# Kernel optimization log

Hardware: AMD Instinct MI355X
Metric: run time of the kernel (lower is better)

## Reference

```python
import jax, jax.numpy as jnp
import numpy as np

R = 25          # regions (hard-coded [:25, 0] slice in the source)
NUM_CONSUMER = 27


def _ln(x, g, b, axes, eps):
    m = jnp.mean(x, axis=axes, keepdims=True)
    v = jnp.mean((x - m) ** 2, axis=axes, keepdims=True)
    return (x - m) / jnp.sqrt(v + eps) * g + b


def setup_inputs() -> dict:
    key = jax.random.key(0)
    n, c, h, e = 64, 64, 8, 1024
    bs = R
    ks = jax.random.split(key, 24)
    inp = {
        "business_structure_target": jax.random.normal(ks[0], (bs, c, n, 4), jnp.float32),
        "business_structure_infected": jax.random.normal(ks[1], (bs, c, n, 4), jnp.float32),
        "customer_structure_target": jax.random.uniform(ks[2], (bs, c, n, NUM_CONSUMER, 4), jnp.float32),
        "customer_structure_infected": jax.random.uniform(ks[3], (bs, c, n, NUM_CONSUMER, 4), jnp.float32),
        "index_target_idx": jax.random.randint(ks[4], (bs, c), 0, R, jnp.int32),
        "index_infected_idx": jax.random.randint(ks[5], (bs, c), 0, R, jnp.int32),
        "covid_outbreak_business": jax.random.randint(ks[6], (bs, c), 0, n, jnp.int32),
        # parameters
        "emb_weight": jax.random.normal(ks[7], (R * n, e), jnp.float32),
        "emb_ln_g": jnp.ones((e,), jnp.float32),
        "emb_ln_b": jnp.zeros((e,), jnp.float32),
        "WQ_t": jax.random.normal(ks[8], (h, e, e), jnp.float32) / np.sqrt(e),
        "WK_t": jax.random.normal(ks[9], (h, e, e), jnp.float32) / np.sqrt(e),
        "WQ_i": jax.random.normal(ks[10], (h, e, e), jnp.float32) / np.sqrt(e),
        "WK_i": jax.random.normal(ks[11], (h, e, e), jnp.float32) / np.sqrt(e),
        "W_os": jax.random.normal(ks[12], (e, e), jnp.float32) / np.sqrt(e),
        "b_os": jnp.zeros((e,), jnp.float32),
        "BS_g": jnp.ones((c, n), jnp.float32), "BS_b": jnp.zeros((c, n), jnp.float32),
        "CS_g": jnp.ones((c, n), jnp.float32), "CS_b": jnp.zeros((c, n), jnp.float32),
        "OS_g": jnp.ones((c, n), jnp.float32), "OS_b": jnp.zeros((c, n), jnp.float32),
    }
    return inp


def _mha(emb_blocks, WQ, WK, indices):
    # emb_blocks: (R, n, e); indices: (d,)
    d = indices.shape[0]
    n, e = emb_blocks.shape[1], emb_blocks.shape[2]
    ew = emb_blocks[indices].reshape(d * n, e)           # gather district blocks
    Q = jnp.einsum('te,hfe->htf', ew, WQ).reshape(-1, d, n, e)  # torch Linear: x @ W.T
    K = jnp.einsum('te,hfe->htf', ew, WK).reshape(-1, d, n, e)
    QK = jnp.einsum('hdie,hdje->hdij', Q, K) / jnp.sqrt(jnp.float32(e))
    # torch Softmax(dim=1) on (d, n, n) -> normalize over the first industry axis
    return jax.nn.softmax(QK, axis=2)                    # (h, d, n, n)


def reference(business_structure_target, business_structure_infected,
              customer_structure_target, customer_structure_infected,
              index_target_idx, index_infected_idx, covid_outbreak_business,
              emb_weight, emb_ln_g, emb_ln_b,
              WQ_t, WK_t, WQ_i, WK_i, W_os, b_os,
              BS_g, BS_b, CS_g, CS_b, OS_g, OS_b):
    n = business_structure_target.shape[2]
    e = emb_weight.shape[1]

    bt = jnp.mean(business_structure_target, -1)[:R, 0]      # (R, n)
    bi = jnp.mean(business_structure_infected, -1)[0]        # (c, n)
    ct = jnp.mean(customer_structure_target, -1)[:R, 0]      # (R, n, 27)
    ci = jnp.mean(customer_structure_infected, -1)[0]        # (c, n, 27)

    emb_norm = _ln(emb_weight, emb_ln_g, emb_ln_b, -1, 1e-16)
    emb_blocks = emb_norm.reshape(R, n, e)

    idx_t = index_target_idx[:R, 0].astype(jnp.int32)        # (R,)
    idx_i = index_infected_idx[0].astype(jnp.int32)          # (c,)

    attn_t = _mha(emb_blocks, WQ_t, WK_t, idx_t)             # (h, R, n, n)
    BR_trg = jnp.einsum('di,hdij->djh', bt, attn_t)          # (R, n, h)
    attn_i = _mha(emb_blocks, WQ_i, WK_i, idx_i)             # (h, c, n, n)
    BR_inf = jnp.einsum('di,hdij->djh', bi, attn_i)          # (c, n, h)

    # cosine similarity over the head dim, broadcast (R,1,n,h) x (1,c,n,h)
    eps = 1e-15
    a = BR_trg[:, None]
    b = BR_inf[None]
    dot = jnp.sum(a * b, -1)
    na = jnp.maximum(jnp.sqrt(jnp.sum(a * a, -1)), eps)
    nb = jnp.maximum(jnp.sqrt(jnp.sum(b * b, -1)), eps)
    BS = dot / (na * nb)                                     # (R, c, n)

    # JSD-style customer-structure similarity
    lt = jax.nn.log_softmax(ct, -1)[:, None]                 # (R, 1, n, 27)
    li = jax.nn.log_softmax(ci, -1)[None]                    # (1, c, n, 27)
    M = jax.nn.log_softmax((lt + li) / 2, -1)
    expM = jnp.exp(M)
    # KLDivLoss(log_target=True): exp(target) * (target - input)
    kl_t = jnp.mean(expM * (M - lt), -1)
    kl_i = jnp.mean(expM * (M - li), -1)
    CS = -((kl_t + kl_i) / 2)                                # (R, c, n)

    # outbreak-business similarity
    cov_buz = covid_outbreak_business[0].astype(jnp.int32)   # (c,)
    inf_emb_idx = idx_i * n + cov_buz
    ob_emb = emb_weight[inf_emb_idx] @ W_os.T + b_os         # (c, e)
    OS = (ob_emb @ emb_weight.T).reshape(-1, R, n)           # (c, R, n)
    OS = jnp.transpose(OS, (1, 0, 2))                        # (R, c, n)

    BS = _ln(BS, BS_g, BS_b, (-2, -1), 1e-5)
    CS = _ln(CS, CS_g, CS_b, (-2, -1), 1e-5)
    OS = _ln(OS, OS_g, OS_b, (-2, -1), 1e-5)
    return (BS, CS, OS)
```

## Files before the change

### kernel.cpp

```cpp
#include <hip/hip_runtime.h>
#include <math.h>

#define RR 25
#define HH 8
#define EE 1024
#define NCN 27

typedef short bf16x8 __attribute__((ext_vector_type(8)));
typedef float f32x4 __attribute__((ext_vector_type(4)));
typedef unsigned short us4 __attribute__((ext_vector_type(4)));
typedef unsigned short us8 __attribute__((ext_vector_type(8)));

__device__ __forceinline__ unsigned short f2bf(float x) {
    union { float f; unsigned int u; } v; v.f = x;
    const unsigned int u = v.u;
    return (unsigned short)((u + 0x7fffu + ((u >> 16) & 1u)) >> 16);
}
__device__ __forceinline__ float bf2f(unsigned short h) {
    union { unsigned int u; float f; } v; v.u = ((unsigned int)h) << 16;
    return v.f;
}

__device__ __forceinline__ float block_reduce_sum_256(float v, float* red) {
#pragma unroll
    for (int off = 32; off > 0; off >>= 1) v += __shfl_down(v, off, 64);
    const int lane = threadIdx.x & 63, wid = threadIdx.x >> 6;
    if (lane == 0) red[wid] = v;
    __syncthreads();
    if (threadIdx.x == 0) red[0] = red[0] + red[1] + red[2] + red[3];
    __syncthreads();
    const float r = red[0];
    __syncthreads();
    return r;
}

__global__ __launch_bounds__(256) void k_ln_emb(
    const float* __restrict__ emb, const float* __restrict__ g,
    const float* __restrict__ b, float* __restrict__ out,
    unsigned short* __restrict__ eh, unsigned short* __restrict__ el)
{
    __shared__ float red[4];
    const int t = blockIdx.x;
    const float* row = emb + (size_t)t * EE;
    float4 x = reinterpret_cast<const float4*>(row)[threadIdx.x];
    float s = x.x + x.y + x.z + x.w;
    s = block_reduce_sum_256(s, red);
    const float m = s * (1.0f / 1024.0f);
    const float d0 = x.x - m, d1 = x.y - m, d2 = x.z - m, d3 = x.w - m;
    float sq = d0*d0 + d1*d1 + d2*d2 + d3*d3;
    sq = block_reduce_sum_256(sq, red);
    const float rs = rsqrtf(sq * (1.0f / 1024.0f) + 1e-16f);
    const float4 gv = reinterpret_cast<const float4*>(g)[threadIdx.x];
    const float4 bv = reinterpret_cast<const float4*>(b)[threadIdx.x];
    float o[4];
    o[0] = d0 * rs * gv.x + bv.x;
    o[1] = d1 * rs * gv.y + bv.y;
    o[2] = d2 * rs * gv.z + bv.z;
    o[3] = d3 * rs * gv.w + bv.w;
    float4 of; of.x = o[0]; of.y = o[1]; of.z = o[2]; of.w = o[3];
    reinterpret_cast<float4*>(out + (size_t)t * EE)[threadIdx.x] = of;
    us4 hv, lv;
#pragma unroll
    for (int j = 0; j < 4; ++j) {
        const unsigned short h = f2bf(o[j]);
        hv[j] = h; lv[j] = f2bf(o[j] - bf2f(h));
    }
    *reinterpret_cast<us4*>(eh + (size_t)t * EE + threadIdx.x * 4) = hv;
    *reinterpret_cast<us4*>(el + (size_t)t * EE + threadIdx.x * 4) = lv;
}

#define WTEN 16777216
#define WPLN 8388608
__global__ __launch_bounds__(256) void k_splitw(
    const float* __restrict__ w0, const float* __restrict__ w1,
    const float* __restrict__ w2, const float* __restrict__ w3,
    unsigned short* __restrict__ wsp)
{
    const int t = blockIdx.y;
    const float* src = (t == 0) ? w0 : ((t == 1) ? w1 : ((t == 2) ? w2 : w3));
    unsigned short* hb = wsp + (size_t)t * WTEN;
    unsigned short* lb = hb + WPLN;
    const size_t q = (size_t)blockIdx.x * 256 + threadIdx.x;
    const float4 x = reinterpret_cast<const float4*>(src)[q];
    const float xf[4] = {x.x, x.y, x.z, x.w};
    us4 hv, lv;
#pragma unroll
    for (int j = 0; j < 4; ++j) {
        const unsigned short h = f2bf(xf[j]);
        hv[j] = h; lv[j] = f2bf(xf[j] - bf2f(h));
    }
    *reinterpret_cast<us4*>(hb + q * 4) = hv;
    *reinterpret_cast<us4*>(lb + q * 4) = lv;
}

struct SplitTiles {
    unsigned short Ah[64][40], Al[64][40], Bh[64][40], Bl[64][40];
};

#define MFMA_COMPUTE(SM)                                                         \
    {                                                                            \
        bf16x8 ah_[2], al_[2], bh_[2], bl_[2];                                   \
        _Pragma("unroll")                                                        \
        for (int m = 0; m < 2; ++m) {                                            \
            const int r = wr * 32 + m * 16 + fr;                                 \
            ah_[m] = *reinterpret_cast<const bf16x8*>(&(SM).Ah[r][ch * 8]);      \
            al_[m] = *reinterpret_cast<const bf16x8*>(&(SM).Al[r][ch * 8]);      \
        }                                                                        \
        _Pragma("unroll")                                                        \
        for (int n = 0; n < 2; ++n) {                                            \
            const int r = wc * 32 + n * 16 + fr;                                 \
            bh_[n] = *reinterpret_cast<const bf16x8*>(&(SM).Bh[r][ch * 8]);      \
            bl_[n] = *reinterpret_cast<const bf16x8*>(&(SM).Bl[r][ch * 8]);      \
        }                                                                        \
        _Pragma("unroll")                                                        \
        for (int m = 0; m < 2; ++m)                                              \
            _Pragma("unroll")                                                    \
            for (int n = 0; n < 2; ++n) {                                        \
                acc[m][n] = __builtin_amdgcn_mfma_f32_16x16x32_bf16(ah_[m], bh_[n], acc[m][n], 0, 0, 0); \
                acc[m][n] = __builtin_amdgcn_mfma_f32_16x16x32_bf16(ah_[m], bl_[n], acc[m][n], 0, 0, 0); \
                acc[m][n] = __builtin_amdgcn_mfma_f32_16x16x32_bf16(al_[m], bh_[n], acc[m][n], 0, 0, 0); \
            }                                                                    \
    }

#define MFMA_STAGE_SPLIT(ABASE, BBASE, SM)                                       \
    {                                                                            \
        float4 ra[2], rb[2];                                                     \
        _Pragma("unroll")                                                        \
        for (int l = 0; l < 2; ++l) {                                            \
            const int id = l * 256 + tid;                                        \
            const int row = id >> 3, c4 = (id & 7) * 4;                          \
            ra[l] = *reinterpret_cast<const float4*>((ABASE) + (size_t)row * EE + k0 + c4); \
            rb[l] = *reinterpret_cast<const float4*>((BBASE) + (size_t)row * EE + k0 + c4); \
        }                                                                        \
        __syncthreads();                                                         \
        _Pragma("unroll")                                                        \
        for (int l = 0; l < 2; ++l) {                                            \
            const int id = l * 256 + tid;                                        \
            const int row = id >> 3, c4 = (id & 7) * 4;                          \
            const float xa[4] = {ra[l].x, ra[l].y, ra[l].z, ra[l].w};            \
            const float xb[4] = {rb[l].x, rb[l].y, rb[l].z, rb[l].w};            \
            us4 ahv, alv, bhv, blv;                                              \
            _Pragma("unroll")                                                    \
            for (int j = 0; j < 4; ++j) {                                        \
                const unsigned short ha = f2bf(xa[j]);                           \
                ahv[j] = ha; alv[j] = f2bf(xa[j] - bf2f(ha));                    \
                const unsigned short hb = f2bf(xb[j]);                           \
                bhv[j] = hb; blv[j] = f2bf(xb[j] - bf2f(hb));                    \
            }                                                                    \
            *reinterpret_cast<us4*>(&(SM).Ah[row][c4]) = ahv;                    \
            *reinterpret_cast<us4*>(&(SM).Al[row][c4]) = alv;                    \
            *reinterpret_cast<us4*>(&(SM).Bh[row][c4]) = bhv;                    \
            *reinterpret_cast<us4*>(&(SM).Bl[row][c4]) = blv;                    \
        }                                                                        \
        __syncthreads();                                                         \
    }

__global__ __launch_bounds__(256) void k_proj_pre(
    const unsigned short* __restrict__ eh, const unsigned short* __restrict__ el,
    const unsigned short* __restrict__ wq, const unsigned short* __restrict__ wk,
    float* __restrict__ Qb, float* __restrict__ Kb, int qkHeadStride)
{
    __shared__ __align__(16) SplitTiles sm;
    const int h = blockIdx.z >> 1;
    const int pk = blockIdx.z & 1;
    const unsigned short* base = pk ? wk : wq;
    const unsigned short* Wh = base + (size_t)h * 1048576;
    const unsigned short* Wl = base + WPLN + (size_t)h * 1048576;
    float* C = (pk ? Kb : Qb) + (size_t)h * qkHeadStride;
    const int bx = blockIdx.x, by = blockIdx.y;
    const int tid = threadIdx.x;
    const int lane = tid & 63, w = tid >> 6;
    const int wr = w >> 1, wc = w & 1;
    const int fr = lane & 15, ch = lane >> 4;
    const int srow = tid >> 2, c8 = (tid & 3) * 8;
    const unsigned short* Ah_src = eh + ((size_t)(by * 64 + srow)) * EE + c8;
    const unsigned short* Al_src = el + ((size_t)(by * 64 + srow)) * EE + c8;
    const unsigned short* Bh_src = Wh + ((size_t)(bx * 64 + srow)) * EE + c8;
    const unsigned short* Bl_src = Wl + ((size_t)(bx * 64 + srow)) * EE + c8;
    f32x4 acc[2][2] = {};
    for (int k0 = 0; k0 < EE; k0 += 32) {
        const us8 va = *reinterpret_cast<const us8*>(Ah_src + k0);
        const us8 vb = *reinterpret_cast<const us8*>(Al_src + k0);
        const us8 vc = *reinterpret_cast<const us8*>(Bh_src + k0);
        const us8 vd = *reinterpret_cast<const us8*>(Bl_src + k0);
        __syncthreads();
        *reinterpret_cast<us8*>(&sm.Ah[srow][c8]) = va;
        *reinterpret_cast<us8*>(&sm.Al[srow][c8]) = vb;
        *reinterpret_cast<us8*>(&sm.Bh[srow][c8]) = vc;
        *reinterpret_cast<us8*>(&sm.Bl[srow][c8]) = vd;
        __syncthreads();
        MFMA_COMPUTE(sm)
    }
    const int rg = lane >> 4;
#pragma unroll
    for (int m = 0; m < 2; ++m)
#pragma unroll
        for (int n = 0; n < 2; ++n)
#pragma unroll
            for (int q = 0; q < 4; ++q) {
                const int row = by * 64 + wr * 32 + m * 16 + rg * 4 + q;
                const int col = bx * 64 + wc * 32 + n * 16 + fr;
                C[(size_t)row * EE + col] = acc[m][n][q];
            }
}

__global__ __launch_bounds__(256) void k_proj_mfma(
    const float* __restrict__ A,
    const float* __restrict__ WQ, const float* __restrict__ WK,
    float* __restrict__ Qb, float* __restrict__ Kb, int qkHeadStride)
{
    __shared__ __align__(16) SplitTiles sm;
    const int h = blockIdx.z >> 1;
    const int pk = blockIdx.z & 1;
    const float* W = (pk ? WK : WQ) + (size_t)h * EE * EE;
    float* C = (pk ? Kb : Qb) + (size_t)h * qkHeadStride;
    const int bx = blockIdx.x, by = blockIdx.y;
    const int tid = threadIdx.x;
    const int lane = tid & 63, w = tid >> 6;
    const int wr = w >> 1, wc = w & 1;
    const int fr = lane & 15, ch = lane >> 4;
    const float* Abase = A + (size_t)by * 64 * EE;
    const float* Bbase = W + (size_t)bx * 64 * EE;
    f32x4 acc[2][2] = {};
    for (int k0 = 0; k0 < EE; k0 += 32) {
        MFMA_STAGE_SPLIT(Abase, Bbase, sm)
        MFMA_COMPUTE(sm)
    }
    const int rg = lane >> 4;
#pragma unroll
    for (int m = 0; m < 2; ++m)
#pragma unroll
        for (int n = 0; n < 2; ++n)
#pragma unroll
            for (int q = 0; q < 4; ++q) {
                const int row = by * 64 + wr * 32 + m * 16 + rg * 4 + q;
                const int col = bx * 64 + wc * 32 + n * 16 + fr;
                C[(size_t)row * EE + col] = acc[m][n][q];
            }
}

__global__ __launch_bounds__(256) void k_qk_mfma(
    const float* __restrict__ Qall, const float* __restrict__ Kall,
    float* __restrict__ attn_all, int qkHeadStride, int attnHeadStride)
{
    __shared__ __align__(16) union { SplitTiles t; float Ss[64][65]; } u;
    __shared__ float redm[4][64];
    __shared__ float reds[4][64];
    const int r = blockIdx.x;
    const int h = blockIdx.y;
    const float* Q = Qall + (size_t)h * qkHeadStride;
    const float* K = Kall + (size_t)h * qkHeadStride;
    float* attn = attn_all + (size_t)h * attnHeadStride + (size_t)r * 4096;
    const int tid = threadIdx.x;
    const int lane = tid & 63, w = tid >> 6;
    const int wr = w >> 1, wc = w & 1;
    const int fr = lane & 15, ch = lane >> 4;
    const float* Abase = Q + (size_t)r * 64 * EE;
    const float* Bbase = K + (size_t)r * 64 * EE;
    f32x4 acc[2][2] = {};
    for (int k0 = 0; k0 < EE; k0 += 32) {
        MFMA_STAGE_SPLIT(Abase, Bbase, u.t)
        MFMA_COMPUTE(u.t)
    }
    __syncthreads();
    const int rg = lane >> 4;
#pragma unroll
    for (int m = 0; m < 2; ++m)
#pragma unroll
        for (int n = 0; n < 2; ++n)
#pragma unroll
            for (int q = 0; q < 4; ++q)
                u.Ss[wr * 32 + m * 16 + rg * 4 + q][wc * 32 + n * 16 + fr] =
                    acc[m][n][q] * (1.0f / 32.0f);
    __syncthreads();
    const int j = tid & 63, seg = tid >> 6;
    float mx = -1e30f;
#pragma unroll
    for (int i = 0; i < 16; ++i) mx = fmaxf(mx, u.Ss[seg * 16 + i][j]);
    redm[seg][j] = mx;
    __syncthreads();
    const float cm = fmaxf(fmaxf(redm[0][j], redm[1][j]), fmaxf(redm[2][j], redm[3][j]));
    float ssum = 0.f;
#pragma unroll
    for (int i = 0; i < 16; ++i) {
        const float e = __expf(u.Ss[seg * 16 + i][j] - cm);
        u.Ss[seg * 16 + i][j] = e;
        ssum += e;
    }
    reds[seg][j] = ssum;
    __syncthreads();
    const float inv = 1.0f / (reds[0][j] + reds[1][j] + reds[2][j] + reds[3][j]);
#pragma unroll
    for (int i = 0; i < 16; ++i)
        attn[(seg * 16 + i) * 64 + j] = u.Ss[seg * 16 + i][j] * inv;
}

#define GEMM_INNER()                                                            \
    _Pragma("unroll 8")                                                         \
    for (int kk = 0; kk < 32; ++kk) {                                           \
        const float a0 = As[ty4+0][kk], a1 = As[ty4+1][kk],                     \
                    a2 = As[ty4+2][kk], a3 = As[ty4+3][kk];                     \
        const float b0 = Bs[tx4+0][kk], b1 = Bs[tx4+1][kk],                     \
                    b2 = Bs[tx4+2][kk], b3 = Bs[tx4+3][kk];                     \
        acc[0][0] += a0*b0; acc[0][1] += a0*b1; acc[0][2] += a0*b2; acc[0][3] += a0*b3; \
        acc[1][0] += a1*b0; acc[1][1] += a1*b1; acc[1][2] += a1*b2; acc[1][3] += a1*b3; \
        acc[2][0] += a2*b0; acc[2][1] += a2*b1; acc[2][2] += a2*b2; acc[2][3] += a2*b3; \
        acc[3][0] += a3*b0; acc[3][1] += a3*b1; acc[3][2] += a3*b2; acc[3][3] += a3*b3; \
    }

#define GEMM_LOAD_TILES(ABASE, BBASE)                                           \
    _Pragma("unroll")                                                           \
    for (int l = 0; l < 2; ++l) {                                               \
        const int idx = l * 256 + tid;                                          \
        const int row = idx >> 3, seg = (idx & 7) * 4;                          \
        const float4 va = *reinterpret_cast<const float4*>((ABASE) + (size_t)row * EE + k0 + seg); \
        As[row][seg+0] = va.x; As[row][seg+1] = va.y;                           \
        As[row][seg+2] = va.z; As[row][seg+3] = va.w;                           \
        const float4 vb = *reinterpret_cast<const float4*>((BBASE) + (size_t)row * EE + k0 + seg); \
        Bs[row][seg+0] = vb.x; Bs[row][seg+1] = vb.y;                           \
        Bs[row][seg+2] = vb.z; Bs[row][seg+3] = vb.w;                           \
    }

__global__ __launch_bounds__(64) void k_br(
    const float* __restrict__ bst, const float* __restrict__ bsi,
    const int* __restrict__ iti, const int* __restrict__ iii,
    const float* __restrict__ attn_t, const float* __restrict__ attn_i,
    float* __restrict__ br_t, float* __restrict__ br_i)
{
    __shared__ float bw[64];
    const int dp = blockIdx.x;
    const int h = blockIdx.y;
    const int j = threadIdx.x;
    const float* attn;
    float* out;
    if (dp < RR) {
        const int d = dp;
        const int rb = iti[d * 64];
        const float* p = bst + ((size_t)(d * 64) * 64 + j) * 4;
        bw[j] = 0.25f * (p[0] + p[1] + p[2] + p[3]);
        attn = attn_t + ((size_t)h * RR + rb) * 4096;
        out = br_t + (size_t)d * 64 * 8;
    } else {
        const int d = dp - RR;
        const int rb = iii[d];
        const float* p = bsi + ((size_t)d * 64 + j) * 4;
        bw[j] = 0.25f * (p[0] + p[1] + p[2] + p[3]);
        attn = attn_i + ((size_t)h * RR + rb) * 4096;
        out = br_i + (size_t)d * 64 * 8;
    }
    __syncthreads();
    float acc = 0.f;
#pragma unroll 8
    for (int i = 0; i < 64; ++i) acc += bw[i] * attn[i * 64 + j];
    out[(size_t)j * 8 + h] = acc;
}

__global__ __launch_bounds__(256) void k_norms(
    const float* __restrict__ br_t, const float* __restrict__ br_i,
    float* __restrict__ na, float* __restrict__ nb)
{
    const int t = blockIdx.x * 256 + threadIdx.x;
    if (t < 1600) {
        float s = 0.f;
#pragma unroll
        for (int h = 0; h < 8; ++h) { const float v = br_t[(size_t)t*8 + h]; s += v*v; }
        na[t] = fmaxf(sqrtf(s), 1e-15f);
    } else if (t < 1600 + 4096) {
        const int u = t - 1600;
        float s = 0.f;
#pragma unroll
        for (int h = 0; h < 8; ++h) { const float v = br_i[(size_t)u*8 + h]; s += v*v; }
        nb[u] = fmaxf(sqrtf(s), 1e-15f);
    }
}

__global__ __launch_bounds__(256) void k_bs(
    const float* __restrict__ br_t, const float* __restrict__ br_i,
    const float* __restrict__ na, const float* __restrict__ nb,
    float* __restrict__ raw)
{
    const int p = blockIdx.x;
#pragma unroll
    for (int it = 0; it < 16; ++it) {
        const int o = it * 256 + threadIdx.x;
        const int q = o >> 6, j = o & 63;
        const float* a = br_t + ((size_t)p * 64 + j) * 8;
        const float* b = br_i + ((size_t)q * 64 + j) * 8;
        float dot = 0.f;
#pragma unroll
        for (int h = 0; h < 8; ++h) dot += a[h] * b[h];
        raw[(size_t)p * 4096 + o] = dot / (na[p * 64 + j] * nb[q * 64 + j]);
    }
}

__global__ __launch_bounds__(256) void k_lsm(
    const float* __restrict__ cst, const float* __restrict__ csi,
    float* __restrict__ lt, float* __restrict__ li)
{
    const int row = blockIdx.x * 256 + threadIdx.x;
    if (row >= 1600 + 4096) return;
    const float* src;
    float* dst;
    if (row < 1600) {
        const int d = row >> 6, i = row & 63;
        src = cst + ((size_t)(d * 64) * 64 + i) * NCN * 4;
        dst = lt + (size_t)row * NCN;
    } else {
        const int u = row - 1600;
        const int q = u >> 6, i = u & 63;
        src = csi + ((size_t)q * 64 + i) * NCN * 4;
        dst = li + (size_t)u * NCN;
    }
    float x[NCN];
    float m = -1e30f;
#pragma unroll
    for (int k = 0; k < NCN; ++k) {
        x[k] = 0.25f * (src[k*4] + src[k*4+1] + src[k*4+2] + src[k*4+3]);
        m = fmaxf(m, x[k]);
    }
    float s = 0.f;
#pragma unroll
    for (int k = 0; k < NCN; ++k) s += __expf(x[k] - m);
    const float lse = m + __logf(s);
#pragma unroll
    for (int k = 0; k < NCN; ++k) dst[k] = x[k] - lse;
}

__global__ __launch_bounds__(256) void k_cs(
    const float* __restrict__ lt, const float* __restrict__ li, float* __restrict__ raw)
{
    const int p = blockIdx.x;
    for (int it = 0; it < 16; ++it) {
        const int o = it * 256 + threadIdx.x;
        const int q = o >> 6, i = o & 63;
        const float* a = lt + ((size_t)p * 64 + i) * NCN;
        const float* b = li + ((size_t)q * 64 + i) * NCN;
        float la[NCN], lb[NCN];
        float m = -1e30f;
#pragma unroll
        for (int k = 0; k < NCN; ++k) {
            la[k] = a[k]; lb[k] = b[k];
            m = fmaxf(m, 0.5f * (la[k] + lb[k]));
        }
        float z = 0.f;
#pragma unroll
        for (int k = 0; k < NCN; ++k) z += __expf(0.5f * (la[k] + lb[k]) - m);
        const float lse = m + __logf(z);
        float kt = 0.f, ki = 0.f;
#pragma unroll
        for (int k = 0; k < NCN; ++k) {
            const float M = 0.5f * (la[k] + lb[k]) - lse;
            const float eM = __expf(M);
            kt += eM * (M - la[k]);
            ki += eM * (M - lb[k]);
        }
        raw[(size_t)p * 4096 + o] = -(kt + ki) * (0.5f / 27.0f);
    }
}

__global__ __launch_bounds__(256) void k_obemb(
    const float* __restrict__ emb, const float* __restrict__ Wos,
    const float* __restrict__ bos, const int* __restrict__ iii,
    const int* __restrict__ cob, float* __restrict__ ob)
{
    __shared__ float As[64][33];
    __shared__ float Bs[64][33];
    __shared__ int gidx[64];
    const int bx = blockIdx.x;
    const int tid = threadIdx.x;
    const int tx = tid & 15, ty = tid >> 4;
    const int ty4 = ty * 4, tx4 = tx * 4;
    if (tid < 64) gidx[tid] = iii[tid] * 64 + cob[tid];
    __syncthreads();
    const float* Bbase = Wos + (size_t)bx * 64 * EE;
    float acc[4][4] = {};
    for (int k0 = 0; k0 < EE; k0 += 32) {
#pragma unroll
        for (int l = 0; l < 2; ++l) {
            const int idx = l * 256 + tid;
            const int row = idx >> 3, seg = (idx & 7) * 4;
            const float4 va = *reinterpret_cast<const float4*>(emb + (size_t)gidx[row] * EE + k0 + seg);
            As[row][seg+0] = va.x; As[row][seg+1] = va.y; As[row][seg+2] = va.z; As[row][seg+3] = va.w;
            const float4 vb = *reinterpret_cast<const float4*>(Bbase + (size_t)row * EE + k0 + seg);
            Bs[row][seg+0] = vb.x; Bs[row][seg+1] = vb.y; Bs[row][seg+2] = vb.z; Bs[row][seg+3] = vb.w;
        }
        __syncthreads();
        GEMM_INNER()
        __syncthreads();
    }
#pragma unroll
    for (int q = 0; q < 4; ++q)
#pragma unroll
        for (int r2 = 0; r2 < 4; ++r2)
            ob[(size_t)(ty4 + q) * EE + bx*64 + tx4 + r2] = acc[q][r2] + bos[bx*64 + tx4 + r2];
}

__global__ __launch_bounds__(256) void k_os(
    const float* __restrict__ ob, const float* __restrict__ emb, float* __restrict__ raw)
{
    __shared__ float As[64][33];
    __shared__ float Bs[64][33];
    const int p = blockIdx.x;
    const int tid = threadIdx.x;
    const int tx = tid & 15, ty = tid >> 4;
    const int ty4 = ty * 4, tx4 = tx * 4;
    const float* Abase = ob;
    const float* Bbase = emb + (size_t)p * 64 * EE;
    float acc[4][4] = {};
    for (int k0 = 0; k0 < EE; k0 += 32) {
        GEMM_LOAD_TILES(Abase, Bbase)
        __syncthreads();
        GEMM_INNER()
        __syncthreads();
    }
#pragma unroll
    for (int q = 0; q < 4; ++q)
#pragma unroll
        for (int r2 = 0; r2 < 4; ++r2)
            raw[(size_t)p * 4096 + (ty4 + q) * 64 + tx4 + r2] = acc[q][r2];
}

__global__ __launch_bounds__(256) void k_final_ln(
    const float* __restrict__ raw,
    const float* __restrict__ BSg, const float* __restrict__ BSb,
    const float* __restrict__ CSg, const float* __restrict__ CSb,
    const float* __restrict__ OSg, const float* __restrict__ OSb,
    float* __restrict__ out)
{
    __shared__ float red[4];
    const int s = blockIdx.x, p = blockIdx.y;
    const float* g  = (s == 0) ? BSg : ((s == 1) ? CSg : OSg);
    const float* bb = (s == 0) ? BSb : ((s == 1) ? CSb : OSb);
    const float* x = raw + ((size_t)s * RR + p) * 4096;
    float v[16];
    float sum = 0.f;
#pragma unroll
    for (int it = 0; it < 16; ++it) { v[it] = x[it * 256 + threadIdx.x]; sum += v[it]; }
    sum = block_reduce_sum_256(sum, red);
    const float m = sum * (1.0f / 4096.0f);
    float sq = 0.f;
#pragma unroll
    for (int it = 0; it < 16; ++it) { const float d = v[it] - m; sq += d * d; }
    sq = block_reduce_sum_256(sq, red);
    const float rs = rsqrtf(sq * (1.0f / 4096.0f) + 1e-5f);
    float* o = out + ((size_t)s * RR + p) * 4096;
#pragma unroll
    for (int it = 0; it < 16; ++it) {
        const int oo = it * 256 + threadIdx.x;
        o[oo] = (v[it] - m) * rs * g[oo] + bb[oo];
    }
}

extern "C" void kernel_launch(void* const* d_in, const int* in_sizes, int n_in,
                              void* d_out, int out_size, void* d_ws, size_t ws_size,
                              hipStream_t stream)
{
    const float* bst = (const float*)d_in[0];
    const float* bsi = (const float*)d_in[1];
    const float* cst = (const float*)d_in[2];
    const float* csi = (const float*)d_in[3];
    const int*   iti = (const int*)d_in[4];
    const int*   iii = (const int*)d_in[5];
    const int*   cob = (const int*)d_in[6];
    const float* embw = (const float*)d_in[7];
    const float* eg  = (const float*)d_in[8];
    const float* ebb = (const float*)d_in[9];
    const float* WQt = (const float*)d_in[10];
    const float* WKt = (const float*)d_in[11];
    const float* WQi = (const float*)d_in[12];
    const float* WKi = (const float*)d_in[13];
    const float* Wos = (const float*)d_in[14];
    const float* bos = (const float*)d_in[15];
    const float* BSg = (const float*)d_in[16];
    const float* BSb = (const float*)d_in[17];
    const float* CSg = (const float*)d_in[18];
    const float* CSb = (const float*)d_in[19];
    const float* OSg = (const float*)d_in[20];
    const float* OSb = (const float*)d_in[21];

    const size_t tailF  = 819200ull*2 + 12800 + 32768 + 1600 + 4096 + 43200 + 110592 + 65536 + 307200;
    const size_t baseF  = 1638400ull + 819200 + 819200;
    const size_t wspF   = 33554432ull;
    const size_t qk8F   = 2ull * 8 * 1600 * EE;
    const size_t qk1F   = 2ull * 1600 * EE;
    const size_t needBig = (baseF + wspF + qk8F + tailF) * 4;
    const size_t needMid = (baseF + qk8F + tailF) * 4;
    const int tier = (ws_size >= needBig) ? 2 : ((ws_size >= needMid) ? 1 : 0);

    float* ws = (float*)d_ws;
    size_t cur = 0;
    float* emb_n = ws + cur;                      cur += 1638400;
    unsigned short* emb_h = (unsigned short*)(ws + cur); cur += 819200;
    unsigned short* emb_l = (unsigned short*)(ws + cur); cur += 819200;
    unsigned short* wsp = nullptr;
    if (tier == 2) { wsp = (unsigned short*)(ws + cur); cur += wspF; }
    const size_t qkSz = (tier >= 1) ? (size_t)8 * 1600 * EE : (size_t)1600 * EE;
    float* Qbuf   = ws + cur;        cur += qkSz;
    float* Kbuf   = ws + cur;        cur += qkSz;
    float* attn_t = ws + cur;        cur += 819200;
    float* attn_i = ws + cur;        cur += 819200;
    float* br_t   = ws + cur;        cur += 12800;
    float* br_i   = ws + cur;        cur += 32768;
    float* na     = ws + cur;        cur += 1600;
    float* nb     = ws + cur;        cur += 4096;
    float* lt     = ws + cur;        cur += 43200;
    float* li     = ws + cur;        cur += 110592;
    float* ob     = ws + cur;        cur += 65536;
    float* raw    = ws + cur;        cur += 307200;

    k_ln_emb<<<1600, 256, 0, stream>>>(embw, eg, ebb, emb_n, emb_h, emb_l);
    if (tier == 2)
        k_splitw<<<dim3(8192, 4), 256, 0, stream>>>(WQt, WKt, WQi, WKi, wsp);

    for (int w = 0; w < 2; ++w) {
        const float* WQ = w ? WQi : WQt;
        const float* WK = w ? WKi : WKt;
        float* attn = w ? attn_i : attn_t;
        if (tier == 2) {
            k_proj_pre<<<dim3(16, 25, 16), 256, 0, stream>>>(
                emb_h, emb_l, wsp + (size_t)(2*w) * WTEN, wsp + (size_t)(2*w+1) * WTEN,
                Qbuf, Kbuf, 1600 * EE);
            k_qk_mfma<<<dim3(25, 8), 256, 0, stream>>>(Qbuf, Kbuf, attn, 1600 * EE, RR * 4096);
        } else if (tier == 1) {
            k_proj_mfma<<<dim3(16, 25, 16), 256, 0, stream>>>(emb_n, WQ, WK, Qbuf, Kbuf, 1600 * EE);
            k_qk_mfma<<<dim3(25, 8), 256, 0, stream>>>(Qbuf, Kbuf, attn, 1600 * EE, RR * 4096);
        } else {
            for (int h = 0; h < HH; ++h) {
                k_proj_mfma<<<dim3(16, 25, 2), 256, 0, stream>>>(
                    emb_n, WQ + (size_t)h * EE * EE, WK + (size_t)h * EE * EE, Qbuf, Kbuf, 0);
                k_qk_mfma<<<dim3(25, 1), 256, 0, stream>>>(
                    Qbuf, Kbuf, attn + (size_t)h * RR * 4096, 0, 0);
            }
        }
    }

    k_br<<<dim3(RR + 64, 8), 64, 0, stream>>>(bst, bsi, iti, iii, attn_t, attn_i, br_t, br_i);
    k_norms<<<23, 256, 0, stream>>>(br_t, br_i, na, nb);
    k_bs<<<25, 256, 0, stream>>>(br_t, br_i, na, nb, raw);
    k_lsm<<<23, 256, 0, stream>>>(cst, csi, lt, li);
    k_cs<<<25, 256, 0, stream>>>(lt, li, raw + 102400);
    k_obemb<<<16, 256, 0, stream>>>(embw, Wos, bos, iii, cob, ob);
    k_os<<<25, 256, 0, stream>>>(ob, embw, raw + 204800);
    k_final_ln<<<dim3(3, RR), 256, 0, stream>>>(raw, BSg, BSb, CSg, CSb, OSg, OSb, (float*)d_out);
}
```

Baseline: 969.2 us.

## Pre-swizzle split-bf16 operands into MFMA fragment layout and enlarge projection tiles

The embedding and weight hi/lo bf16 splits are now written directly in per-lane MFMA fragment order. A new projection kernel loads contiguous slabs into LDS with no padding or transposition and computes a 64x256 tile per block, with a block-to-XCD mapping for L2 locality. This targets the operand re-fetch and LDS staging overhead of the dominant Q/K projection GEMMs. It also folds the norm kernel into k_bs and moves the small outbreak GEMMs from scalar FMA to split-bf16 MFMA, which raises register pressure and may lower occupancy.

```diff
diff --git a/kernel.cpp b/kernel.cpp
--- a/kernel.cpp
+++ b/kernel.cpp
@@ -34,10 +34,13 @@
     return r;
 }
 
+#define WTEN 16777216ull
+#define WHEAD 2097152ull
+
 __global__ __launch_bounds__(256) void k_ln_emb(
     const float* __restrict__ emb, const float* __restrict__ g,
     const float* __restrict__ b, float* __restrict__ out,
-    unsigned short* __restrict__ eh, unsigned short* __restrict__ el)
+    unsigned short* __restrict__ Apl)
 {
     __shared__ float red[4];
     const int t = blockIdx.x;
@@ -65,12 +68,14 @@
         const unsigned short h = f2bf(o[j]);
         hv[j] = h; lv[j] = f2bf(o[j] - bf2f(h));
     }
-    *reinterpret_cast<us4*>(eh + (size_t)t * EE + threadIdx.x * 4) = hv;
-    *reinterpret_cast<us4*>(el + (size_t)t * EE + threadIdx.x * 4) = lv;
-}
-
-#define WTEN 16777216
-#define WPLN 8388608
+    const int k0 = threadIdx.x * 4;
+    const int kt = k0 >> 5, kc = (k0 >> 3) & 3, j0 = k0 & 7;
+    const int lane = (t & 15) + 16 * kc;
+    const size_t base = ((size_t)(kt * 100 + (t >> 4)) * 2) * 512 + lane * 8 + j0;
+    *reinterpret_cast<us4*>(Apl + base)       = hv;
+    *reinterpret_cast<us4*>(Apl + base + 512) = lv;
+}
+
 __global__ __launch_bounds__(256) void k_splitw(
     const float* __restrict__ w0, const float* __restrict__ w1,
     const float* __restrict__ w2, const float* __restrict__ w3,
@@ -78,8 +83,7 @@
 {
     const int t = blockIdx.y;
     const float* src = (t == 0) ? w0 : ((t == 1) ? w1 : ((t == 2) ? w2 : w3));
-    unsigned short* hb = wsp + (size_t)t * WTEN;
-    unsigned short* lb = hb + WPLN;
+    unsigned short* dst = wsp + (size_t)t * WTEN;
     const size_t q = (size_t)blockIdx.x * 256 + threadIdx.x;
     const float4 x = reinterpret_cast<const float4*>(src)[q];
     const float xf[4] = {x.x, x.y, x.z, x.w};
@@ -89,8 +93,85 @@
         const unsigned short h = f2bf(xf[j]);
         hv[j] = h; lv[j] = f2bf(xf[j] - bf2f(h));
     }
-    *reinterpret_cast<us4*>(hb + q * 4) = hv;
-    *reinterpret_cast<us4*>(lb + q * 4) = lv;
+    const size_t e4 = q * 4;
+    const int h = (int)(e4 >> 20);
+    const int rem = (int)(e4 & 1048575);
+    const int f = rem >> 10, e = rem & 1023;
+    const int kt = e >> 5, kc = (e >> 3) & 3, j0 = e & 7;
+    const int lane = (f & 15) + 16 * kc;
+    const size_t base = (size_t)h * WHEAD + ((size_t)(kt * 64 + (f >> 4)) * 2) * 512 + lane * 8 + j0;
+    *reinterpret_cast<us4*>(dst + base)       = hv;
+    *reinterpret_cast<us4*>(dst + base + 512) = lv;
+}
+
+__global__ __launch_bounds__(256) void k_proj2(
+    const unsigned short* __restrict__ Apl,
+    const unsigned short* __restrict__ Wpl,
+    float* __restrict__ Qb, float* __restrict__ Kb)
+{
+    __shared__ __align__(16) unsigned short As_l[8 * 512];
+    __shared__ __align__(16) unsigned short Bs_l[32 * 512];
+    const int fid = blockIdx.x;
+    const int xcd = fid & 7;
+    const int iw = fid >> 3;
+    const int z = xcd + (iw / 100) * 8;
+    const int mb = iw % 100;
+    const int by = mb >> 2, bx = mb & 3;
+    const int pk = z >> 3, h = z & 7;
+    const unsigned short* Wb = Wpl + (size_t)pk * WTEN + (size_t)h * WHEAD;
+    float* C = (pk ? Kb : Qb) + (size_t)h * 1600 * EE;
+    const int tid = threadIdx.x;
+    const int lane = tid & 63, wv = tid >> 6;
+    const int by4 = by * 4, bx16 = bx * 16;
+    f32x4 acc[4][4] = {};
+    for (int kt = 0; kt < 32; ++kt) {
+        const unsigned short* aslab = Apl + ((size_t)(kt * 100 + by4)) * 1024;
+        const unsigned short* bslab = Wb  + ((size_t)(kt * 64  + bx16)) * 1024;
+        us8 ra0 = *reinterpret_cast<const us8*>(aslab + (size_t)tid * 8);
+        us8 ra1 = *reinterpret_cast<const us8*>(aslab + (size_t)(256 + tid) * 8);
+        us8 rb[8];
+#pragma unroll
+        for (int c = 0; c < 8; ++c)
+            rb[c] = *reinterpret_cast<const us8*>(bslab + (size_t)(c * 256 + tid) * 8);
+        __syncthreads();
+        *reinterpret_cast<us8*>(As_l + tid * 8) = ra0;
+        *reinterpret_cast<us8*>(As_l + (256 + tid) * 8) = ra1;
+#pragma unroll
+        for (int c = 0; c < 8; ++c)
+            *reinterpret_cast<us8*>(Bs_l + (c * 256 + tid) * 8) = rb[c];
+        __syncthreads();
+        bf16x8 ah[4], al[4], bh[4], bl[4];
+#pragma unroll
+        for (int m = 0; m < 4; ++m) {
+            ah[m] = *reinterpret_cast<const bf16x8*>(As_l + (m * 2 + 0) * 512 + lane * 8);
+            al[m] = *reinterpret_cast<const bf16x8*>(As_l + (m * 2 + 1) * 512 + lane * 8);
+        }
+#pragma unroll
+        for (int n = 0; n < 4; ++n) {
+            const int nt = wv * 4 + n;
+            bh[n] = *reinterpret_cast<const bf16x8*>(Bs_l + (nt * 2 + 0) * 512 + lane * 8);
+            bl[n] = *reinterpret_cast<const bf16x8*>(Bs_l + (nt * 2 + 1) * 512 + lane * 8);
+        }
+#pragma unroll
+        for (int m = 0; m < 4; ++m)
+#pragma unroll
+            for (int n = 0; n < 4; ++n) {
+                acc[m][n] = __builtin_amdgcn_mfma_f32_16x16x32_bf16(ah[m], bh[n], acc[m][n], 0, 0, 0);
+                acc[m][n] = __builtin_amdgcn_mfma_f32_16x16x32_bf16(ah[m], bl[n], acc[m][n], 0, 0, 0);
+                acc[m][n] = __builtin_amdgcn_mfma_f32_16x16x32_bf16(al[m], bh[n], acc[m][n], 0, 0, 0);
+            }
+    }
+    const int rg = lane >> 4, fr = lane & 15;
+#pragma unroll
+    for (int m = 0; m < 4; ++m)
+#pragma unroll
+        for (int n = 0; n < 4; ++n)
+#pragma unroll
+            for (int q = 0; q < 4; ++q) {
+                const int row = by * 64 + m * 16 + rg * 4 + q;
+                const int col = bx * 256 + wv * 64 + n * 16 + fr;
+                C[(size_t)row * EE + col] = acc[m][n][q];
+            }
 }
 
 struct SplitTiles {
@@ -122,15 +203,15 @@
             }                                                                    \
     }
 
-#define MFMA_STAGE_SPLIT(ABASE, BBASE, SM)                                       \
+#define MFMA_STAGE_SPLIT_GEN(AROW, BROW, SM)                                     \
     {                                                                            \
         float4 ra[2], rb[2];                                                     \
         _Pragma("unroll")                                                        \
         for (int l = 0; l < 2; ++l) {                                            \
             const int id = l * 256 + tid;                                        \
             const int row = id >> 3, c4 = (id & 7) * 4;                          \
-            ra[l] = *reinterpret_cast<const float4*>((ABASE) + (size_t)row * EE + k0 + c4); \
-            rb[l] = *reinterpret_cast<const float4*>((BBASE) + (size_t)row * EE + k0 + c4); \
+            ra[l] = *reinterpret_cast<const float4*>((AROW(row)) + k0 + c4);     \
+            rb[l] = *reinterpret_cast<const float4*>((BROW(row)) + k0 + c4);     \
         }                                                                        \
         __syncthreads();                                                         \
         _Pragma("unroll")                                                        \
@@ -155,55 +236,6 @@
         __syncthreads();                                                         \
     }
 
-__global__ __launch_bounds__(256) void k_proj_pre(
-    const unsigned short* __restrict__ eh, const unsigned short* __restrict__ el,
-    const unsigned short* __restrict__ wq, const unsigned short* __restrict__ wk,
-    float* __restrict__ Qb, float* __restrict__ Kb, int qkHeadStride)
-{
-    __shared__ __align__(16) SplitTiles sm;
-    const int h = blockIdx.z >> 1;
-    const int pk = blockIdx.z & 1;
-    const unsigned short* base = pk ? wk : wq;
-    const unsigned short* Wh = base + (size_t)h * 1048576;
-    const unsigned short* Wl = base + WPLN + (size_t)h * 1048576;
-    float* C = (pk ? Kb : Qb) + (size_t)h * qkHeadStride;
-    const int bx = blockIdx.x, by = blockIdx.y;
-    const int tid = threadIdx.x;
-    const int lane = tid & 63, w = tid >> 6;
-    const int wr = w >> 1, wc = w & 1;
-    const int fr = lane & 15, ch = lane >> 4;
-    const int srow = tid >> 2, c8 = (tid & 3) * 8;
-    const unsigned short* Ah_src = eh + ((size_t)(by * 64 + srow)) * EE + c8;
-    const unsigned short* Al_src = el + ((size_t)(by * 64 + srow)) * EE + c8;
-    const unsigned short* Bh_src = Wh + ((size_t)(bx * 64 + srow)) * EE + c8;
-    const unsigned short* Bl_src = Wl + ((size_t)(bx * 64 + srow)) * EE + c8;
-    f32x4 acc[2][2] = {};
-    for (int k0 = 0; k0 < EE; k0 += 32) {
-        const us8 va = *reinterpret_cast<const us8*>(Ah_src + k0);
-        const us8 vb = *reinterpret_cast<const us8*>(Al_src + k0);
-        const us8 vc = *reinterpret_cast<const us8*>(Bh_src + k0);
-        const us8 vd = *reinterpret_cast<const us8*>(Bl_src + k0);
-        __syncthreads();
-        *reinterpret_cast<us8*>(&sm.Ah[srow][c8]) = va;
-        *reinterpret_cast<us8*>(&sm.Al[srow][c8]) = vb;
-        *reinterpret_cast<us8*>(&sm.Bh[srow][c8]) = vc;
-        *reinterpret_cast<us8*>(&sm.Bl[srow][c8]) = vd;
-        __syncthreads();
-        MFMA_COMPUTE(sm)
-    }
-    const int rg = lane >> 4;
-#pragma unroll
-    for (int m = 0; m < 2; ++m)
-#pragma unroll
-        for (int n = 0; n < 2; ++n)
-#pragma unroll
-            for (int q = 0; q < 4; ++q) {
-                const int row = by * 64 + wr * 32 + m * 16 + rg * 4 + q;
-                const int col = bx * 64 + wc * 32 + n * 16 + fr;
-                C[(size_t)row * EE + col] = acc[m][n][q];
-            }
-}
-
 __global__ __launch_bounds__(256) void k_proj_mfma(
     const float* __restrict__ A,
     const float* __restrict__ WQ, const float* __restrict__ WK,
@@ -221,11 +253,15 @@
     const int fr = lane & 15, ch = lane >> 4;
     const float* Abase = A + (size_t)by * 64 * EE;
     const float* Bbase = W + (size_t)bx * 64 * EE;
+#define AROWP(r) (Abase + (size_t)(r) * EE)
+#define BROWP(r) (Bbase + (size_t)(r) * EE)
     f32x4 acc[2][2] = {};
     for (int k0 = 0; k0 < EE; k0 += 32) {
-        MFMA_STAGE_SPLIT(Abase, Bbase, sm)
+        MFMA_STAGE_SPLIT_GEN(AROWP, BROWP, sm)
         MFMA_COMPUTE(sm)
     }
+#undef AROWP
+#undef BROWP
     const int rg = lane >> 4;
 #pragma unroll
     for (int m = 0; m < 2; ++m)
@@ -257,11 +293,15 @@
     const int fr = lane & 15, ch = lane >> 4;
     const float* Abase = Q + (size_t)r * 64 * EE;
     const float* Bbase = K + (size_t)r * 64 * EE;
+#define AROWP(rr) (Abase + (size_t)(rr) * EE)
+#define BROWP(rr) (Bbase + (size_t)(rr) * EE)
     f32x4 acc[2][2] = {};
     for (int k0 = 0; k0 < EE; k0 += 32) {
-        MFMA_STAGE_SPLIT(Abase, Bbase, u.t)
+        MFMA_STAGE_SPLIT_GEN(AROWP, BROWP, u.t)
         MFMA_COMPUTE(u.t)
     }
+#undef AROWP
+#undef BROWP
     __syncthreads();
     const int rg = lane >> 4;
 #pragma unroll
@@ -294,32 +334,6 @@
     for (int i = 0; i < 16; ++i)
         attn[(seg * 16 + i) * 64 + j] = u.Ss[seg * 16 + i][j] * inv;
 }
-
-#define GEMM_INNER()                                                            \
-    _Pragma("unroll 8")                                                         \
-    for (int kk = 0; kk < 32; ++kk) {                                           \
-        const float a0 = As[ty4+0][kk], a1 = As[ty4+1][kk],                     \
-                    a2 = As[ty4+2][kk], a3 = As[ty4+3][kk];                     \
-        const float b0 = Bs[tx4+0][kk], b1 = Bs[tx4+1][kk],                     \
-                    b2 = Bs[tx4+2][kk], b3 = Bs[tx4+3][kk];                     \
-        acc[0][0] += a0*b0; acc[0][1] += a0*b1; acc[0][2] += a0*b2; acc[0][3] += a0*b3; \
-        acc[1][0] += a1*b0; acc[1][1] += a1*b1; acc[1][2] += a1*b2; acc[1][3] += a1*b3; \
-        acc[2][0] += a2*b0; acc[2][1] += a2*b1; acc[2][2] += a2*b2; acc[2][3] += a2*b3; \
-        acc[3][0] += a3*b0; acc[3][1] += a3*b1; acc[3][2] += a3*b2; acc[3][3] += a3*b3; \
-    }
-
-#define GEMM_LOAD_TILES(ABASE, BBASE)                                           \
-    _Pragma("unroll")                                                           \
-    for (int l = 0; l < 2; ++l) {                                               \
-        const int idx = l * 256 + tid;                                          \
-        const int row = idx >> 3, seg = (idx & 7) * 4;                          \
-        const float4 va = *reinterpret_cast<const float4*>((ABASE) + (size_t)row * EE + k0 + seg); \
-        As[row][seg+0] = va.x; As[row][seg+1] = va.y;                           \
-        As[row][seg+2] = va.z; As[row][seg+3] = va.w;                           \
-        const float4 vb = *reinterpret_cast<const float4*>((BBASE) + (size_t)row * EE + k0 + seg); \
-        Bs[row][seg+0] = vb.x; Bs[row][seg+1] = vb.y;                           \
-        Bs[row][seg+2] = vb.z; Bs[row][seg+3] = vb.w;                           \
-    }
 
 __global__ __launch_bounds__(64) void k_br(
     const float* __restrict__ bst, const float* __restrict__ bsi,
@@ -355,28 +369,8 @@
     out[(size_t)j * 8 + h] = acc;
 }
 
-__global__ __launch_bounds__(256) void k_norms(
-    const float* __restrict__ br_t, const float* __restrict__ br_i,
-    float* __restrict__ na, float* __restrict__ nb)
-{
-    const int t = blockIdx.x * 256 + threadIdx.x;
-    if (t < 1600) {
-        float s = 0.f;
-#pragma unroll
-        for (int h = 0; h < 8; ++h) { const float v = br_t[(size_t)t*8 + h]; s += v*v; }
-        na[t] = fmaxf(sqrtf(s), 1e-15f);
-    } else if (t < 1600 + 4096) {
-        const int u = t - 1600;
-        float s = 0.f;
-#pragma unroll
-        for (int h = 0; h < 8; ++h) { const float v = br_i[(size_t)u*8 + h]; s += v*v; }
-        nb[u] = fmaxf(sqrtf(s), 1e-15f);
-    }
-}
-
 __global__ __launch_bounds__(256) void k_bs(
     const float* __restrict__ br_t, const float* __restrict__ br_i,
-    const float* __restrict__ na, const float* __restrict__ nb,
     float* __restrict__ raw)
 {
     const int p = blockIdx.x;
@@ -386,10 +380,15 @@
         const int q = o >> 6, j = o & 63;
         const float* a = br_t + ((size_t)p * 64 + j) * 8;
         const float* b = br_i + ((size_t)q * 64 + j) * 8;
-        float dot = 0.f;
-#pragma unroll
-        for (int h = 0; h < 8; ++h) dot += a[h] * b[h];
-        raw[(size_t)p * 4096 + o] = dot / (na[p * 64 + j] * nb[q * 64 + j]);
+        float dot = 0.f, sa = 0.f, sb = 0.f;
+#pragma unroll
+        for (int h = 0; h < 8; ++h) {
+            const float va = a[h], vb = b[h];
+            dot += va * vb; sa += va * va; sb += vb * vb;
+        }
+        const float na = fmaxf(sqrtf(sa), 1e-15f);
+        const float nb = fmaxf(sqrtf(sb), 1e-15f);
+        raw[(size_t)p * 4096 + o] = dot / (na * nb);
     }
 }
 
@@ -458,66 +457,73 @@
     }
 }
 
-__global__ __launch_bounds__(256) void k_obemb(
+__global__ __launch_bounds__(256) void k_obemb2(
     const float* __restrict__ emb, const float* __restrict__ Wos,
     const float* __restrict__ bos, const int* __restrict__ iii,
     const int* __restrict__ cob, float* __restrict__ ob)
 {
-    __shared__ float As[64][33];
-    __shared__ float Bs[64][33];
+    __shared__ __align__(16) SplitTiles sm;
     __shared__ int gidx[64];
     const int bx = blockIdx.x;
     const int tid = threadIdx.x;
-    const int tx = tid & 15, ty = tid >> 4;
-    const int ty4 = ty * 4, tx4 = tx * 4;
+    const int lane = tid & 63, w = tid >> 6;
+    const int wr = w >> 1, wc = w & 1;
+    const int fr = lane & 15, ch = lane >> 4;
     if (tid < 64) gidx[tid] = iii[tid] * 64 + cob[tid];
     __syncthreads();
     const float* Bbase = Wos + (size_t)bx * 64 * EE;
-    float acc[4][4] = {};
+#define AROWP(r) (emb + (size_t)gidx[(r)] * EE)
+#define BROWP(r) (Bbase + (size_t)(r) * EE)
+    f32x4 acc[2][2] = {};
     for (int k0 = 0; k0 < EE; k0 += 32) {
-#pragma unroll
-        for (int l = 0; l < 2; ++l) {
-            const int idx = l * 256 + tid;
-            const int row = idx >> 3, seg = (idx & 7) * 4;
-            const float4 va = *reinterpret_cast<const float4*>(emb + (size_t)gidx[row] * EE + k0 + seg);
-            As[row][seg+0] = va.x; As[row][seg+1] = va.y; As[row][seg+2] = va.z; As[row][seg+3] = va.w;
-            const float4 vb = *reinterpret_cast<const float4*>(Bbase + (size_t)row * EE + k0 + seg);
-            Bs[row][seg+0] = vb.x; Bs[row][seg+1] = vb.y; Bs[row][seg+2] = vb.z; Bs[row][seg+3] = vb.w;
-        }
-        __syncthreads();
-        GEMM_INNER()
-        __syncthreads();
-    }
-#pragma unroll
-    for (int q = 0; q < 4; ++q)
-#pragma unroll
-        for (int r2 = 0; r2 < 4; ++r2)
-            ob[(size_t)(ty4 + q) * EE + bx*64 + tx4 + r2] = acc[q][r2] + bos[bx*64 + tx4 + r2];
-}
-
-__global__ __launch_bounds__(256) void k_os(
+        MFMA_STAGE_SPLIT_GEN(AROWP, BROWP, sm)
+        MFMA_COMPUTE(sm)
+    }
+#undef AROWP
+#undef BROWP
+    const int rg = lane >> 4;
+#pragma unroll
+    for (int m = 0; m < 2; ++m)
+#pragma unroll
+        for (int n = 0; n < 2; ++n)
+#pragma unroll
+            for (int q = 0; q < 4; ++q) {
+                const int row = wr * 32 + m * 16 + rg * 4 + q;
+                const int col = bx * 64 + wc * 32 + n * 16 + fr;
+                ob[(size_t)row * EE + col] = acc[m][n][q] + bos[col];
+            }
+}
+
+__global__ __launch_bounds__(256) void k_os2(
     const float* __restrict__ ob, const float* __restrict__ emb, float* __restrict__ raw)
 {
-    __shared__ float As[64][33];
-    __shared__ float Bs[64][33];
+    __shared__ __align__(16) SplitTiles sm;
     const int p = blockIdx.x;
     const int tid = threadIdx.x;
-    const int tx = tid & 15, ty = tid >> 4;
-    const int ty4 = ty * 4, tx4 = tx * 4;
-    const float* Abase = ob;
+    const int lane = tid & 63, w = tid >> 6;
+    const int wr = w >> 1, wc = w & 1;
+    const int fr = lane & 15, ch = lane >> 4;
     const float* Bbase = emb + (size_t)p * 64 * EE;
-    float acc[4][4] = {};
+#define AROWP(r) (ob + (size_t)(r) * EE)
+#define BROWP(r) (Bbase + (size_t)(r) * EE)
+    f32x4 acc[2][2] = {};
     for (int k0 = 0; k0 < EE; k0 += 32) {
-        GEMM_LOAD_TILES(Abase, Bbase)
-        __syncthreads();
-        GEMM_INNER()
-        __syncthreads();
-    }
-#pragma unroll
-    for (int q = 0; q < 4; ++q)
-#pragma unroll
-        for (int r2 = 0; r2 < 4; ++r2)
-            raw[(size_t)p * 4096 + (ty4 + q) * 64 + tx4 + r2] = acc[q][r2];
+        MFMA_STAGE_SPLIT_GEN(AROWP, BROWP, sm)
+        MFMA_COMPUTE(sm)
+    }
+#undef AROWP
+#undef BROWP
+    const int rg = lane >> 4;
+#pragma unroll
+    for (int m = 0; m < 2; ++m)
+#pragma unroll
+        for (int n = 0; n < 2; ++n)
+#pragma unroll
+            for (int q = 0; q < 4; ++q) {
+                const int row = wr * 32 + m * 16 + rg * 4 + q;
+                const int col = wc * 32 + n * 16 + fr;
+                raw[(size_t)p * 4096 + row * 64 + col] = acc[m][n][q];
+            }
 }
 
 __global__ __launch_bounds__(256) void k_final_ln(
@@ -578,22 +584,20 @@
     const float* OSg = (const float*)d_in[20];
     const float* OSb = (const float*)d_in[21];
 
-    const size_t tailF  = 819200ull*2 + 12800 + 32768 + 1600 + 4096 + 43200 + 110592 + 65536 + 307200;
-    const size_t baseF  = 1638400ull + 819200 + 819200;
+    const size_t tailF  = 819200ull*2 + 12800 + 32768 + 43200 + 110592 + 65536 + 307200;
+    const size_t baseF  = 1638400ull + 1638400;
     const size_t wspF   = 33554432ull;
     const size_t qk8F   = 2ull * 8 * 1600 * EE;
-    const size_t qk1F   = 2ull * 1600 * EE;
     const size_t needBig = (baseF + wspF + qk8F + tailF) * 4;
     const size_t needMid = (baseF + qk8F + tailF) * 4;
     const int tier = (ws_size >= needBig) ? 2 : ((ws_size >= needMid) ? 1 : 0);
 
     float* ws = (float*)d_ws;
     size_t cur = 0;
-    float* emb_n = ws + cur;                      cur += 1638400;
-    unsigned short* emb_h = (unsigned short*)(ws + cur); cur += 819200;
-    unsigned short* emb_l = (unsigned short*)(ws + cur); cur += 819200;
+    float* emb_n = ws + cur;                               cur += 1638400;
+    unsigned short* Apl = (unsigned short*)(ws + cur);     cur += 1638400;
     unsigned short* wsp = nullptr;
-    if (tier == 2) { wsp = (unsigned short*)(ws + cur); cur += wspF; }
+    if (tier == 2) { wsp = (unsigned short*)(ws + cur);    cur += wspF; }
     const size_t qkSz = (tier >= 1) ? (size_t)8 * 1600 * EE : (size_t)1600 * EE;
     float* Qbuf   = ws + cur;        cur += qkSz;
     float* Kbuf   = ws + cur;        cur += qkSz;
@@ -601,14 +605,12 @@
     float* attn_i = ws + cur;        cur += 819200;
     float* br_t   = ws + cur;        cur += 12800;
     float* br_i   = ws + cur;        cur += 32768;
-    float* na     = ws + cur;        cur += 1600;
-    float* nb     = ws + cur;        cur += 4096;
     float* lt     = ws + cur;        cur += 43200;
     float* li     = ws + cur;        cur += 110592;
     float* ob     = ws + cur;        cur += 65536;
     float* raw    = ws + cur;        cur += 307200;
 
-    k_ln_emb<<<1600, 256, 0, stream>>>(embw, eg, ebb, emb_n, emb_h, emb_l);
+    k_ln_emb<<<1600, 256, 0, stream>>>(embw, eg, ebb, emb_n, Apl);
     if (tier == 2)
         k_splitw<<<dim3(8192, 4), 256, 0, stream>>>(WQt, WKt, WQi, WKi, wsp);
 
@@ -617,9 +619,7 @@
         const float* WK = w ? WKi : WKt;
         float* attn = w ? attn_i : attn_t;
         if (tier == 2) {
-            k_proj_pre<<<dim3(16, 25, 16), 256, 0, stream>>>(
-                emb_h, emb_l, wsp + (size_t)(2*w) * WTEN, wsp + (size_t)(2*w+1) * WTEN,
-                Qbuf, Kbuf, 1600 * EE);
+            k_proj2<<<1600, 256, 0, stream>>>(Apl, wsp + (size_t)(2*w) * WTEN, Qbuf, Kbuf);
             k_qk_mfma<<<dim3(25, 8), 256, 0, stream>>>(Qbuf, Kbuf, attn, 1600 * EE, RR * 4096);
         } else if (tier == 1) {
             k_proj_mfma<<<dim3(16, 25, 16), 256, 0, stream>>>(emb_n, WQ, WK, Qbuf, Kbuf, 1600 * EE);
@@ -635,11 +635,10 @@
     }
 
     k_br<<<dim3(RR + 64, 8), 64, 0, stream>>>(bst, bsi, iti, iii, attn_t, attn_i, br_t, br_i);
-    k_norms<<<23, 256, 0, stream>>>(br_t, br_i, na, nb);
-    k_bs<<<25, 256, 0, stream>>>(br_t, br_i, na, nb, raw);
+    k_bs<<<25, 256, 0, stream>>>(br_t, br_i, raw);
     k_lsm<<<23, 256, 0, stream>>>(cst, csi, lt, li);
     k_cs<<<25, 256, 0, stream>>>(lt, li, raw + 102400);
-    k_obemb<<<16, 256, 0, stream>>>(embw, Wos, bos, iii, cob, ob);
-    k_os<<<25, 256, 0, stream>>>(ob, embw, raw + 204800);
+    k_obemb2<<<16, 256, 0, stream>>>(embw, Wos, bos, iii, cob, ob);
+    k_os2<<<25, 256, 0, stream>>>(ob, embw, raw + 204800);
     k_final_ln<<<dim3(3, RR), 256, 0, stream>>>(raw, BSg, BSb, CSg, CSb, OSg, OSb, (float*)d_out);
 }
```

Measured after the change: 862.0 us. -11.1%, faster.
